# Kernel tuning notes

Hardware: AMD Instinct MI355X
Metric: run time of the kernel (lower is better)

The kernel has to match this reference:

```python
import jax, jax.numpy as jnp
import numpy as np

N, NFEAT, NHID1, NHID2, NCLASS = 16384, 512, 256, 128, 8


def setup_inputs() -> dict:
    key = jax.random.key(0)
    ks = jax.random.split(key, 8)
    x = jax.random.normal(ks[0], (N, NFEAT), dtype=jnp.float32)
    adj = jax.random.uniform(ks[1], (N, N), dtype=jnp.float32)
    W1 = jax.random.normal(ks[2], (NFEAT, NHID1), dtype=jnp.float32) * (1.0 / np.sqrt(NFEAT))
    b1 = jnp.zeros((NHID1,), dtype=jnp.float32)
    W2 = jax.random.normal(ks[3], (NHID1, NHID2), dtype=jnp.float32) * (1.0 / np.sqrt(NHID1))
    b2 = jnp.zeros((NHID2,), dtype=jnp.float32)
    W3 = jax.random.normal(ks[4], (NHID2, NCLASS), dtype=jnp.float32) * (1.0 / np.sqrt(NHID2))
    b3 = jnp.zeros((NCLASS,), dtype=jnp.float32)
    return {"x": x, "adj": adj, "W1": W1, "b1": b1, "W2": W2, "b2": b2, "W3": W3, "b3": b3}


def _gc(x, adj, W, b):
    # GraphConvolution (Kipf): support = x @ W; out = adj @ support + b
    return adj @ (x @ W) + b


def reference(x, adj, W1, b1, W2, b2, W3, b3):
    # eval mode: dropout is identity
    h = jax.nn.relu(_gc(x, adj, W1, b1))
    h = jax.nn.relu(_gc(h, adj, W2, b2))
    h = _gc(h, adj, W3, b3)
    return jax.nn.log_softmax(h, axis=1)
```

## Files before the change

kernel.cpp:

```cpp
#include <hip/hip_runtime.h>
#include <hip/hip_bf16.h>

#define NROW 16384
#define NFEATC 512
#define NH1 256
#define NH2 128
#define NCLS 8

typedef __attribute__((ext_vector_type(8))) short short8;
typedef __attribute__((ext_vector_type(4))) float f32x4;

__device__ __forceinline__ ushort f2bf(float f) {
  union { float f; unsigned u; } v; v.f = f;
  unsigned r = v.u + 0x7FFFu + ((v.u >> 16) & 1u);
  return (ushort)(r >> 16);
}
__device__ __forceinline__ float bf2f(ushort h) {
  union { unsigned u; float f; } v; v.u = ((unsigned)h) << 16; return v.f;
}

__device__ __forceinline__ void gl_lds16(const ushort* g, ushort* l) {
  __builtin_amdgcn_global_load_lds(
      (const __attribute__((address_space(1))) unsigned int*)g,
      (__attribute__((address_space(3))) unsigned int*)l, 16, 0, 0);
}

__global__ __launch_bounds__(256) void transpose_conv(
    const float* __restrict__ in, ushort* __restrict__ out, int K, int N) {
  int idx = blockIdx.x * 256 + threadIdx.x;
  if (idx < K * N) {
    int k = idx / N, n = idx % N;
    out[(size_t)n * K + k] = f2bf(in[idx]);
  }
}

template<int BM, int BN, int WM, int WN, int KSPLIT, bool AFP32, int OUTM, bool WADJ, int MINW>
__global__ __launch_bounds__(256, MINW) void gemm_pipe(
    const void* __restrict__ Ap, const ushort* __restrict__ BT,
    void* __restrict__ Outp, ushort* __restrict__ adjBF,
    const float* __restrict__ bias,
    const int nm, const int nn, const int M, const int N, const int K)
{
  constexpr int BK = 64, LDSK = BK + 8;
  constexpr int MR = WM / 16, NR = WN / 16;
  constexpr int nWc = BN / WN;
  static_assert((BM / WM) * (BN / WN) == 4, "4 waves");
  constexpr int AELEM = BM * BK / 256, ATPR = BK / AELEM;
  constexpr int BELEM = BN * BK / 256, BTPR = BK / BELEM;
  constexpr int A4s = AFP32 ? AELEM / 4 : 1;
  constexpr int A8s = AFP32 ? 1 : AELEM / 8;
  constexpr int B8s = (BELEM >= 8) ? BELEM / 8 : 1;

  __shared__ ushort As[2][BM * LDSK];
  __shared__ ushort Bs[2][BN * LDSK];

  const int t = threadIdx.x, l = t & 63, wid = t >> 6;
  const int wr0 = (wid / nWc) * WM, wc0 = (wid % nWc) * WN;

  const int cpx = gridDim.x >> 3;
  const int flat = (blockIdx.x & 7) * cpx + (blockIdx.x >> 3);
  const int n_blk = flat % nn;
  const int m_blk = (flat / nn) % nm;
  const int ksl = flat / (nn * nm);
  const int bm0 = m_blk * BM, bn0 = n_blk * BN;
  const int kper = K / KSPLIT, kbase = ksl * kper;
  const int NT = kper / BK;

  const int ar = t / ATPR, ak = (t % ATPR) * AELEM;
  const int br = t / BTPR, bk = (t % BTPR) * BELEM;

  const float*  Af = (const float*)Ap + (size_t)(bm0 + ar) * K + kbase + ak;
  const ushort* Ab = (const ushort*)Ap + (size_t)(bm0 + ar) * K + kbase + ak;
  const ushort* Bp = BT + (size_t)(bn0 + br) * K + kbase + bk;
  ushort* adjW = WADJ ? (adjBF + (size_t)(bm0 + ar) * K + kbase + ak) : nullptr;
  const bool wbf = WADJ && (n_blk == 0);

  f32x4 acc[MR][NR] = {};

  float4 aF[A4s];
  short8 aB[A8s];
  short8 bV[B8s];
  ushort4 b4;

  auto loadRegs = [&](int it) {
    const int ko = it * BK;
    if constexpr (AFP32) {
      #pragma unroll
      for (int c = 0; c < A4s; c++) aF[c] = *(const float4*)(Af + ko + 4 * c);
    } else {
      #pragma unroll
      for (int c = 0; c < A8s; c++) aB[c] = *(const short8*)(Ab + ko + 8 * c);
    }
    if constexpr (BELEM >= 8) {
      #pragma unroll
      for (int c = 0; c < B8s; c++) bV[c] = *(const short8*)(Bp + ko + 8 * c);
    } else {
      b4 = *(const ushort4*)(Bp + ko);
    }
  };

  auto writeLds = [&](int buf, int it) {
    const int ko = it * BK;
    if constexpr (AFP32) {
      #pragma unroll
      for (int c = 0; c < A4s; c++) {
        ushort4 v;
        v.x = f2bf(aF[c].x); v.y = f2bf(aF[c].y);
        v.z = f2bf(aF[c].z); v.w = f2bf(aF[c].w);
        *(ushort4*)&As[buf][ar * LDSK + ak + 4 * c] = v;
        if (wbf) *(ushort4*)(adjW + ko + 4 * c) = v;
      }
    } else {
      #pragma unroll
      for (int c = 0; c < A8s; c++)
        *(short8*)&As[buf][ar * LDSK + ak + 8 * c] = aB[c];
    }
    if constexpr (BELEM >= 8) {
      #pragma unroll
      for (int c = 0; c < B8s; c++)
        *(short8*)&Bs[buf][br * LDSK + bk + 8 * c] = bV[c];
    } else {
      *(ushort4*)&Bs[buf][br * LDSK + bk] = b4;
    }
  };

  auto compute = [&](int buf) {
    const int rr = l & 15;
    #pragma unroll
    for (int kk = 0; kk < 2; kk++) {
      const int kb = kk * 32 + (l >> 4) * 8;
      short8 af[MR], bfv[NR];
      #pragma unroll
      for (int m = 0; m < MR; m++)
        af[m] = *(short8*)&As[buf][(wr0 + m * 16 + rr) * LDSK + kb];
      #pragma unroll
      for (int n = 0; n < NR; n++)
        bfv[n] = *(short8*)&Bs[buf][(wc0 + n * 16 + rr) * LDSK + kb];
      #pragma unroll
      for (int m = 0; m < MR; m++)
        #pragma unroll
        for (int n = 0; n < NR; n++)
          acc[m][n] = __builtin_amdgcn_mfma_f32_16x16x32_bf16(af[m], bfv[n], acc[m][n], 0, 0, 0);
    }
  };

  loadRegs(0);
  writeLds(0, 0);
  __syncthreads();
  for (int it = 0; it < NT; it++) {
    const int cur = it & 1;
    if (it + 1 < NT) loadRegs(it + 1);
    compute(cur);
    if (it + 1 < NT) writeLds(cur ^ 1, it + 1);
    __syncthreads();
  }

  #pragma unroll
  for (int m = 0; m < MR; m++) {
    const int row = bm0 + wr0 + m * 16 + (l >> 4) * 4;
    #pragma unroll
    for (int n = 0; n < NR; n++) {
      const int col = bn0 + wc0 + n * 16 + (l & 15);
      if constexpr (OUTM == 1) {
        ushort4 v;
        v.x = f2bf(acc[m][n][0]); v.y = f2bf(acc[m][n][1]);
        v.z = f2bf(acc[m][n][2]); v.w = f2bf(acc[m][n][3]);
        *(ushort4*)((ushort*)Outp + (size_t)col * M + row) = v;
      } else if constexpr (OUTM == 2) {
        float* o = (float*)Outp + (size_t)ksl * M * N;
        #pragma unroll
        for (int r = 0; r < 4; r++)
          o[(size_t)(row + r) * N + col] = acc[m][n][r];
      } else {
        const float bv = bias[col];
        ushort* o = (ushort*)Outp;
        #pragma unroll
        for (int r = 0; r < 4; r++)
          o[(size_t)(row + r) * N + col] = f2bf(fmaxf(acc[m][n][r] + bv, 0.0f));
      }
    }
  }
}

template<int BN, int KSPLIT, int MINW>
__global__ __launch_bounds__(256, MINW) void gemm_lds(
    const ushort* __restrict__ A, const ushort* __restrict__ BT,
    float* __restrict__ part, const int nm, const int M, const int N, const int K)
{
  constexpr int BM = 128, BK = 64;
  constexpr int WM = (BN >= 64) ? 64 : 32;
  constexpr int WN = (BN >= 64) ? 64 : BN;
  constexpr int MR = WM / 16, NR = WN / 16;
  constexpr int nWc = BN / WN;
  __shared__ ushort As[BM * BK];
  __shared__ ushort Bs[BN * BK];

  const int t = threadIdx.x, l = t & 63, wid = t >> 6;
  const int rr = l & 15, hi = l >> 4, r7 = rr & 7;
  const int rin = l >> 3, cin = l & 7;
  const int wr0 = (wid / nWc) * WM, wc0 = (wid % nWc) * WN;

  const int cpx = gridDim.x >> 3;
  const int flat = (blockIdx.x & 7) * cpx + (blockIdx.x >> 3);
  const int m_blk = flat % nm;
  const int ksl  = flat / nm;
  const int bm0 = m_blk * BM;
  const int kper = K / KSPLIT, kbase = ksl * kper;
  const int NT = kper / BK;

  f32x4 acc[MR][NR] = {};

  const int scol = 8 * (cin ^ rin);
  const ushort* Arow[4];
  #pragma unroll
  for (int a = 0; a < 4; a++) {
    const int row = (wid * 4 + a) * 8 + rin;
    Arow[a] = A + (size_t)(bm0 + row) * K + kbase + scol;
  }
  const ushort* Brow[(BN == 128) ? 4 : 1];
  if constexpr (BN == 128) {
    #pragma unroll
    for (int a = 0; a < 4; a++) {
      const int row = (wid * 4 + a) * 8 + rin;
      Brow[a] = BT + (size_t)row * K + kbase + scol;
    }
  } else {
    const int row = wid * 8 + rin;
    Brow[0] = BT + (size_t)row * K + kbase + scol;
  }

  for (int it = 0; it < NT; it++) {
    const int ko = it * BK;
    #pragma unroll
    for (int a = 0; a < 4; a++)
      gl_lds16(Arow[a] + ko, &As[(wid * 4 + a) * 512]);
    if constexpr (BN == 128) {
      #pragma unroll
      for (int a = 0; a < 4; a++)
        gl_lds16(Brow[a] + ko, &Bs[(wid * 4 + a) * 512]);
    } else {
      if (wid < 2) gl_lds16(Brow[0] + ko, &Bs[wid * 512]);
    }
    __syncthreads();
    #pragma unroll
    for (int kk = 0; kk < 2; kk++) {
      const int cof = 8 * ((kk * 4 + hi) ^ r7);
      short8 af[MR], bfv[NR];
      #pragma unroll
      for (int m = 0; m < MR; m++)
        af[m] = *(const short8*)&As[(wr0 + m * 16 + rr) * 64 + cof];
      #pragma unroll
      for (int n = 0; n < NR; n++)
        bfv[n] = *(const short8*)&Bs[(wc0 + n * 16 + rr) * 64 + cof];
      #pragma unroll
      for (int m = 0; m < MR; m++)
        #pragma unroll
        for (int n = 0; n < NR; n++)
          acc[m][n] = __builtin_amdgcn_mfma_f32_16x16x32_bf16(af[m], bfv[n], acc[m][n], 0, 0, 0);
    }
    __syncthreads();
  }

  float* o = part + (size_t)ksl * M * N;
  #pragma unroll
  for (int m = 0; m < MR; m++) {
    const int row = bm0 + wr0 + m * 16 + hi * 4;
    #pragma unroll
    for (int n = 0; n < NR; n++) {
      const int col = wc0 + n * 16 + rr;
      #pragma unroll
      for (int r = 0; r < 4; r++)
        o[(size_t)(row + r) * N + col] = acc[m][n][r];
    }
  }
}

__global__ __launch_bounds__(256) void reduce_relu(
    const float* __restrict__ part, const float* __restrict__ bias,
    ushort* __restrict__ out, const int MN, const int N, const int KS) {
  const int i4 = (blockIdx.x * 256 + threadIdx.x) * 4;
  if (i4 >= MN) return;
  float4 s = *(const float4*)(part + i4);
  for (int k = 1; k < KS; k++) {
    float4 p = *(const float4*)(part + (size_t)k * MN + i4);
    s.x += p.x; s.y += p.y; s.z += p.z; s.w += p.w;
  }
  const int col = i4 % N;
  float4 b = *(const float4*)(bias + col);
  ushort4 v;
  v.x = f2bf(fmaxf(s.x + b.x, 0.0f));
  v.y = f2bf(fmaxf(s.y + b.y, 0.0f));
  v.z = f2bf(fmaxf(s.z + b.z, 0.0f));
  v.w = f2bf(fmaxf(s.w + b.w, 0.0f));
  *(ushort4*)(out + i4) = v;
}

__global__ __launch_bounds__(64) void mm_small(
    const ushort* __restrict__ h2, const float* __restrict__ W3,
    ushort* __restrict__ s3T) {
  __shared__ float w[NH2 * NCLS];
  for (int i = threadIdx.x; i < NH2 * NCLS; i += 64) w[i] = W3[i];
  __syncthreads();
  const int m = blockIdx.x * 64 + threadIdx.x;
  float acc[8] = {};
  const ushort* row = h2 + (size_t)m * NH2;
  #pragma unroll
  for (int c = 0; c < NH2 / 8; c++) {
    short8 v = *(const short8*)(row + c * 8);
    #pragma unroll
    for (int j = 0; j < 8; j++) {
      float h = bf2f((ushort)v[j]);
      const int k = c * 8 + j;
      #pragma unroll
      for (int n = 0; n < 8; n++) acc[n] += h * w[k * 8 + n];
    }
  }
  #pragma unroll
  for (int n = 0; n < 8; n++) s3T[(size_t)n * NROW + m] = f2bf(acc[n]);
  #pragma unroll
  for (int n = 8; n < 16; n++) s3T[(size_t)n * NROW + m] = 0;
}

__global__ __launch_bounds__(256) void final_reduce(
    const float* __restrict__ part, const float* __restrict__ b3,
    float* __restrict__ out) {
  const int m = blockIdx.x * 256 + threadIdx.x;
  float4 s0 = make_float4(0, 0, 0, 0), s1 = make_float4(0, 0, 0, 0);
  #pragma unroll
  for (int k = 0; k < 4; k++) {
    const float4* p = (const float4*)(part + ((size_t)k * NROW + m) * 16);
    float4 a = p[0], b = p[1];
    s0.x += a.x; s0.y += a.y; s0.z += a.z; s0.w += a.w;
    s1.x += b.x; s1.y += b.y; s1.z += b.z; s1.w += b.w;
  }
  float v[8];
  v[0] = s0.x + b3[0]; v[1] = s0.y + b3[1]; v[2] = s0.z + b3[2]; v[3] = s0.w + b3[3];
  v[4] = s1.x + b3[4]; v[5] = s1.y + b3[5]; v[6] = s1.z + b3[6]; v[7] = s1.w + b3[7];
  float mx = v[0];
  #pragma unroll
  for (int n = 1; n < 8; n++) mx = fmaxf(mx, v[n]);
  float s = 0.0f;
  #pragma unroll
  for (int n = 0; n < 8; n++) s += expf(v[n] - mx);
  const float lse = logf(s) + mx;
  float4* o = (float4*)(out + (size_t)m * 8);
  o[0] = make_float4(v[0] - lse, v[1] - lse, v[2] - lse, v[3] - lse);
  o[1] = make_float4(v[4] - lse, v[5] - lse, v[6] - lse, v[7] - lse);
}

extern "C" void kernel_launch(void* const* d_in, const int* in_sizes, int n_in,
                              void* d_out, int out_size, void* d_ws, size_t ws_size,
                              hipStream_t stream) {
  const float* x   = (const float*)d_in[0];
  const float* adj = (const float*)d_in[1];
  const float* W1  = (const float*)d_in[2];
  const float* b1  = (const float*)d_in[3];
  const float* W2  = (const float*)d_in[4];
  const float* b2  = (const float*)d_in[5];
  const float* W3  = (const float*)d_in[6];
  const float* b3  = (const float*)d_in[7];
  float* out = (float*)d_out;

  char* ws = (char*)d_ws;
  size_t off = 0;
  ushort* W1T = (ushort*)(ws + off); off += (size_t)NH1 * NFEATC * 2;
  ushort* W2T = (ushort*)(ws + off); off += (size_t)NH2 * NH1 * 2;
  ushort* s1T = (ushort*)(ws + off); off += (size_t)NH1 * NROW * 2;
  ushort* h1  = (ushort*)(ws + off); off += (size_t)NROW * NH1 * 2;
  ushort* s2T = (ushort*)(ws + off); off += (size_t)NH2 * NROW * 2;
  ushort* h2  = (ushort*)(ws + off); off += (size_t)NROW * NH2 * 2;
  ushort* s3T = (ushort*)(ws + off); off += (size_t)16 * NROW * 2;
  float*  part = (float*)(ws + off); off += (size_t)4 * NROW * NH2 * 4;
  ushort* adjBF = (ushort*)(ws + off); off += (size_t)NROW * NROW * 2;

  transpose_conv<<<(NFEATC * NH1 + 255) / 256, 256, 0, stream>>>(W1, W1T, NFEATC, NH1);
  transpose_conv<<<(NH1 * NH2 + 255) / 256, 256, 0, stream>>>(W2, W2T, NH1, NH2);

  gemm_pipe<64, 128, 32, 64, 1, true, 1, false, 2><<<512, 256, 0, stream>>>(
      x, W1T, s1T, nullptr, nullptr, 256, 2, NROW, NH1, NFEATC);
  gemm_pipe<128, 128, 64, 64, 2, true, 2, true, 2><<<512, 256, 0, stream>>>(
      adj, s1T, part, adjBF, nullptr, 128, 2, NROW, NH1, NROW);
  reduce_relu<<<NROW * NH1 / 4 / 256, 256, 0, stream>>>(
      part, b1, h1, NROW * NH1, NH1, 2);
  gemm_pipe<64, 128, 32, 64, 1, false, 1, false, 2><<<256, 256, 0, stream>>>(
      h1, W2T, s2T, nullptr, nullptr, 256, 1, NROW, NH2, NH1);
  gemm_lds<128, 4, 4><<<512, 256, 0, stream>>>(
      adjBF, s2T, part, 128, NROW, NH2, NROW);
  reduce_relu<<<NROW * NH2 / 4 / 256, 256, 0, stream>>>(
      part, b2, h2, NROW * NH2, NH2, 4);
  mm_small<<<NROW / 64, 64, 0, stream>>>(h2, W3, s3T);
  gemm_lds<16, 4, 4><<<512, 256, 0, stream>>>(
      adjBF, s3T, part, 128, NROW, 16, NROW);
  final_reduce<<<NROW / 256, 256, 0, stream>>>(part, b3, out);
}
```

Before: 894.9 us.

## Double-buffer LDS in adjacency GEMMs, add dedicated fp32-adj convert GEMM, reverse K order

Replaces the generic fp32 adjacency GEMM with a specialized gemm_cvt kernel. It uses swizzled LDS, async global-to-LDS loads for the B operand, and wider 16-byte bf16 stores of the converted adjacency. The gemm_lds kernels become double-buffered with prefetch of the next K tile, and the layer-2 pass walks K in reverse to reuse adjacency data still in cache from the previous pass. The layer-3 pass doubles its K split to 8 with more blocks, so final_reduce sums 8 partials. The aim is to overlap loads with MFMA work and improve L2/MALL reuse, at the cost of more LDS per block and lower occupancy.

```diff
diff --git a/kernel.cpp b/kernel.cpp
--- a/kernel.cpp
+++ b/kernel.cpp
@@ -34,11 +34,10 @@
   }
 }
 
-template<int BM, int BN, int WM, int WN, int KSPLIT, bool AFP32, int OUTM, bool WADJ, int MINW>
+template<int BM, int BN, int WM, int WN, int KSPLIT, bool AFP32, int OUTM, int MINW>
 __global__ __launch_bounds__(256, MINW) void gemm_pipe(
     const void* __restrict__ Ap, const ushort* __restrict__ BT,
-    void* __restrict__ Outp, ushort* __restrict__ adjBF,
-    const float* __restrict__ bias,
+    void* __restrict__ Outp, const float* __restrict__ bias,
     const int nm, const int nn, const int M, const int N, const int K)
 {
   constexpr int BK = 64, LDSK = BK + 8;
@@ -72,8 +71,6 @@
   const float*  Af = (const float*)Ap + (size_t)(bm0 + ar) * K + kbase + ak;
   const ushort* Ab = (const ushort*)Ap + (size_t)(bm0 + ar) * K + kbase + ak;
   const ushort* Bp = BT + (size_t)(bn0 + br) * K + kbase + bk;
-  ushort* adjW = WADJ ? (adjBF + (size_t)(bm0 + ar) * K + kbase + ak) : nullptr;
-  const bool wbf = WADJ && (n_blk == 0);
 
   f32x4 acc[MR][NR] = {};
 
@@ -99,8 +96,7 @@
     }
   };
 
-  auto writeLds = [&](int buf, int it) {
-    const int ko = it * BK;
+  auto writeLds = [&](int buf) {
     if constexpr (AFP32) {
       #pragma unroll
       for (int c = 0; c < A4s; c++) {
@@ -108,7 +104,6 @@
         v.x = f2bf(aF[c].x); v.y = f2bf(aF[c].y);
         v.z = f2bf(aF[c].z); v.w = f2bf(aF[c].w);
         *(ushort4*)&As[buf][ar * LDSK + ak + 4 * c] = v;
-        if (wbf) *(ushort4*)(adjW + ko + 4 * c) = v;
       }
     } else {
       #pragma unroll
@@ -145,13 +140,13 @@
   };
 
   loadRegs(0);
-  writeLds(0, 0);
+  writeLds(0);
   __syncthreads();
   for (int it = 0; it < NT; it++) {
     const int cur = it & 1;
     if (it + 1 < NT) loadRegs(it + 1);
     compute(cur);
-    if (it + 1 < NT) writeLds(cur ^ 1, it + 1);
+    if (it + 1 < NT) writeLds(cur ^ 1);
     __syncthreads();
   }
 
@@ -166,11 +161,6 @@
         v.x = f2bf(acc[m][n][0]); v.y = f2bf(acc[m][n][1]);
         v.z = f2bf(acc[m][n][2]); v.w = f2bf(acc[m][n][3]);
         *(ushort4*)((ushort*)Outp + (size_t)col * M + row) = v;
-      } else if constexpr (OUTM == 2) {
-        float* o = (float*)Outp + (size_t)ksl * M * N;
-        #pragma unroll
-        for (int r = 0; r < 4; r++)
-          o[(size_t)(row + r) * N + col] = acc[m][n][r];
       } else {
         const float bv = bias[col];
         ushort* o = (ushort*)Outp;
@@ -182,8 +172,8 @@
   }
 }
 
-template<int BN, int KSPLIT, int MINW>
-__global__ __launch_bounds__(256, MINW) void gemm_lds(
+template<int BN, int KSPLIT, bool KREV, int MINW>
+__global__ __launch_bounds__(256, MINW) void gemm_lds2(
     const ushort* __restrict__ A, const ushort* __restrict__ BT,
     float* __restrict__ part, const int nm, const int M, const int N, const int K)
 {
@@ -192,8 +182,8 @@
   constexpr int WN = (BN >= 64) ? 64 : BN;
   constexpr int MR = WM / 16, NR = WN / 16;
   constexpr int nWc = BN / WN;
-  __shared__ ushort As[BM * BK];
-  __shared__ ushort Bs[BN * BK];
+  __shared__ ushort As[2][BM * BK];
+  __shared__ ushort Bs[2][BN * BK];
 
   const int t = threadIdx.x, l = t & 63, wid = t >> 6;
   const int rr = l & 15, hi = l >> 4, r7 = rr & 7;
@@ -203,7 +193,7 @@
   const int cpx = gridDim.x >> 3;
   const int flat = (blockIdx.x & 7) * cpx + (blockIdx.x >> 3);
   const int m_blk = flat % nm;
-  const int ksl  = flat / nm;
+  const int ksl = flat / nm;
   const int bm0 = m_blk * BM;
   const int kper = K / KSPLIT, kbase = ksl * kper;
   const int NT = kper / BK;
@@ -213,51 +203,55 @@
   const int scol = 8 * (cin ^ rin);
   const ushort* Arow[4];
   #pragma unroll
+  for (int a = 0; a < 4; a++)
+    Arow[a] = A + (size_t)(bm0 + (wid * 4 + a) * 8 + rin) * K + kbase + scol;
+  const ushort* Brow[4];
+  #pragma unroll
   for (int a = 0; a < 4; a++) {
-    const int row = (wid * 4 + a) * 8 + rin;
-    Arow[a] = A + (size_t)(bm0 + row) * K + kbase + scol;
-  }
-  const ushort* Brow[(BN == 128) ? 4 : 1];
-  if constexpr (BN == 128) {
-    #pragma unroll
-    for (int a = 0; a < 4; a++) {
-      const int row = (wid * 4 + a) * 8 + rin;
-      Brow[a] = BT + (size_t)row * K + kbase + scol;
-    }
-  } else {
-    const int row = wid * 8 + rin;
-    Brow[0] = BT + (size_t)row * K + kbase + scol;
-  }
-
-  for (int it = 0; it < NT; it++) {
-    const int ko = it * BK;
+    int row = (BN == 128) ? ((wid * 4 + a) * 8 + rin) : (wid * 8 + rin);
+    if (row >= BN) row = 0;
+    Brow[a] = BT + (size_t)row * K + kbase + scol;
+  }
+
+  auto STAGE = [&](int buf, int it) {
+    const int ko = (KREV ? (NT - 1 - it) : it) * BK;
     #pragma unroll
     for (int a = 0; a < 4; a++)
-      gl_lds16(Arow[a] + ko, &As[(wid * 4 + a) * 512]);
+      gl_lds16(Arow[a] + ko, &As[buf][(wid * 4 + a) * 512]);
     if constexpr (BN == 128) {
       #pragma unroll
       for (int a = 0; a < 4; a++)
-        gl_lds16(Brow[a] + ko, &Bs[(wid * 4 + a) * 512]);
+        gl_lds16(Brow[a] + ko, &Bs[buf][(wid * 4 + a) * 512]);
     } else {
-      if (wid < 2) gl_lds16(Brow[0] + ko, &Bs[wid * 512]);
-    }
-    __syncthreads();
+      if (wid < 2) gl_lds16(Brow[0] + ko, &Bs[buf][wid * 512]);
+    }
+  };
+
+  auto COMPUTE = [&](int buf) {
     #pragma unroll
     for (int kk = 0; kk < 2; kk++) {
       const int cof = 8 * ((kk * 4 + hi) ^ r7);
       short8 af[MR], bfv[NR];
       #pragma unroll
       for (int m = 0; m < MR; m++)
-        af[m] = *(const short8*)&As[(wr0 + m * 16 + rr) * 64 + cof];
+        af[m] = *(const short8*)&As[buf][(wr0 + m * 16 + rr) * 64 + cof];
       #pragma unroll
       for (int n = 0; n < NR; n++)
-        bfv[n] = *(const short8*)&Bs[(wc0 + n * 16 + rr) * 64 + cof];
+        bfv[n] = *(const short8*)&Bs[buf][(wc0 + n * 16 + rr) * 64 + cof];
       #pragma unroll
       for (int m = 0; m < MR; m++)
         #pragma unroll
         for (int n = 0; n < NR; n++)
           acc[m][n] = __builtin_amdgcn_mfma_f32_16x16x32_bf16(af[m], bfv[n], acc[m][n], 0, 0, 0);
     }
+  };
+
+  STAGE(0, 0);
+  __syncthreads();
+  for (int it = 0; it < NT; it++) {
+    const int cur = it & 1;
+    if (it + 1 < NT) STAGE(cur ^ 1, it + 1);
+    COMPUTE(cur);
     __syncthreads();
   }
 
@@ -271,6 +265,109 @@
       #pragma unroll
       for (int r = 0; r < 4; r++)
         o[(size_t)(row + r) * N + col] = acc[m][n][r];
+    }
+  }
+}
+
+__global__ __launch_bounds__(256, 2) void gemm_cvt(
+    const float* __restrict__ adj, const ushort* __restrict__ BT,
+    float* __restrict__ part, ushort* __restrict__ adjBF)
+{
+  constexpr int BM = 128, BN = 128, BK = 64, MR = 4, NR = 4;
+  __shared__ ushort As[2][BM * BK];
+  __shared__ ushort Bs[2][BN * BK];
+
+  const int t = threadIdx.x, l = t & 63, wid = t >> 6;
+  const int rr = l & 15, hi = l >> 4, r7 = rr & 7;
+  const int rin = l >> 3, cin = l & 7;
+  const int wr0 = (wid >> 1) * 64, wc0 = (wid & 1) * 64;
+
+  const int cpx = gridDim.x >> 3;
+  const int flat = (blockIdx.x & 7) * cpx + (blockIdx.x >> 3);
+  const int n_blk = flat & 1;
+  const int m_blk = (flat >> 1) & 127;
+  const int ksl = flat >> 8;
+  const int bm0 = m_blk * BM, bn0 = n_blk * BN;
+  const int kbase = ksl * (NROW / 2);
+  constexpr int NT = (NROW / 2) / BK;
+
+  const int ar = t >> 1;
+  const int ac4 = (t & 1) * 4;
+  const float* Af = adj + (size_t)(bm0 + ar) * NROW + kbase + ac4 * 8;
+  ushort* adjW = adjBF + (size_t)(bm0 + ar) * NROW + kbase + ac4 * 8;
+  const bool wbf = (n_blk == 0);
+
+  const int scol = 8 * (cin ^ rin);
+  const ushort* Brow[4];
+  #pragma unroll
+  for (int a = 0; a < 4; a++)
+    Brow[a] = BT + (size_t)(bn0 + (wid * 4 + a) * 8 + rin) * NROW + kbase + scol;
+
+  f32x4 acc[MR][NR] = {};
+  float4 aF[8];
+
+  auto LOADA = [&](int it) {
+    #pragma unroll
+    for (int c = 0; c < 8; c++) aF[c] = *(const float4*)(Af + it * 64 + c * 4);
+  };
+  auto STAGEB = [&](int buf, int it) {
+    #pragma unroll
+    for (int a = 0; a < 4; a++)
+      gl_lds16(Brow[a] + it * 64, &Bs[buf][(wid * 4 + a) * 512]);
+  };
+  auto WRITEA = [&](int buf, int it) {
+    #pragma unroll
+    for (int j = 0; j < 4; j++) {
+      short8 v;
+      v[0] = (short)f2bf(aF[2 * j].x);     v[1] = (short)f2bf(aF[2 * j].y);
+      v[2] = (short)f2bf(aF[2 * j].z);     v[3] = (short)f2bf(aF[2 * j].w);
+      v[4] = (short)f2bf(aF[2 * j + 1].x); v[5] = (short)f2bf(aF[2 * j + 1].y);
+      v[6] = (short)f2bf(aF[2 * j + 1].z); v[7] = (short)f2bf(aF[2 * j + 1].w);
+      *(short8*)&As[buf][ar * 64 + 8 * ((ac4 + j) ^ (ar & 7))] = v;
+      if (wbf) *(short8*)(adjW + it * 64 + j * 8) = v;
+    }
+  };
+  auto COMPUTE = [&](int buf) {
+    #pragma unroll
+    for (int kk = 0; kk < 2; kk++) {
+      const int cof = 8 * ((kk * 4 + hi) ^ r7);
+      short8 af[MR], bfv[NR];
+      #pragma unroll
+      for (int m = 0; m < MR; m++)
+        af[m] = *(const short8*)&As[buf][(wr0 + m * 16 + rr) * 64 + cof];
+      #pragma unroll
+      for (int n = 0; n < NR; n++)
+        bfv[n] = *(const short8*)&Bs[buf][(wc0 + n * 16 + rr) * 64 + cof];
+      #pragma unroll
+      for (int m = 0; m < MR; m++)
+        #pragma unroll
+        for (int n = 0; n < NR; n++)
+          acc[m][n] = __builtin_amdgcn_mfma_f32_16x16x32_bf16(af[m], bfv[n], acc[m][n], 0, 0, 0);
+    }
+  };
+
+  LOADA(0);
+  STAGEB(0, 0);
+  WRITEA(0, 0);
+  __syncthreads();
+  for (int it = 0; it < NT; it++) {
+    const int cur = it & 1;
+    if (it + 1 < NT) { LOADA(it + 1); STAGEB(cur ^ 1, it + 1); }
+    COMPUTE(cur);
+    if (it + 1 < NT) WRITEA(cur ^ 1, it + 1);
+    __syncthreads();
+  }
+
+  float* o = part + (size_t)ksl * NROW * NH1;
+  #pragma unroll
+  for (int m = 0; m < MR; m++) {
+    const int row = bm0 + wr0 + m * 16 + hi * 4;
+    #pragma unroll
+    for (int n = 0; n < NR; n++) {
+      const int col = bn0 + wc0 + n * 16 + rr;
+      #pragma unroll
+      for (int r = 0; r < 4; r++)
+        o[(size_t)(row + r) * NH1 + col] = acc[m][n][r];
     }
   }
 }
@@ -327,7 +424,7 @@
   const int m = blockIdx.x * 256 + threadIdx.x;
   float4 s0 = make_float4(0, 0, 0, 0), s1 = make_float4(0, 0, 0, 0);
   #pragma unroll
-  for (int k = 0; k < 4; k++) {
+  for (int k = 0; k < 8; k++) {
     const float4* p = (const float4*)(part + ((size_t)k * NROW + m) * 16);
     float4 a = p[0], b = p[1];
     s0.x += a.x; s0.y += a.y; s0.z += a.z; s0.w += a.w;
@@ -370,26 +467,25 @@
   ushort* s2T = (ushort*)(ws + off); off += (size_t)NH2 * NROW * 2;
   ushort* h2  = (ushort*)(ws + off); off += (size_t)NROW * NH2 * 2;
   ushort* s3T = (ushort*)(ws + off); off += (size_t)16 * NROW * 2;
-  float*  part = (float*)(ws + off); off += (size_t)4 * NROW * NH2 * 4;
+  float*  part = (float*)(ws + off); off += (size_t)2 * NROW * NH1 * 4;
   ushort* adjBF = (ushort*)(ws + off); off += (size_t)NROW * NROW * 2;
 
   transpose_conv<<<(NFEATC * NH1 + 255) / 256, 256, 0, stream>>>(W1, W1T, NFEATC, NH1);
   transpose_conv<<<(NH1 * NH2 + 255) / 256, 256, 0, stream>>>(W2, W2T, NH1, NH2);
 
-  gemm_pipe<64, 128, 32, 64, 1, true, 1, false, 2><<<512, 256, 0, stream>>>(
-      x, W1T, s1T, nullptr, nullptr, 256, 2, NROW, NH1, NFEATC);
-  gemm_pipe<128, 128, 64, 64, 2, true, 2, true, 2><<<512, 256, 0, stream>>>(
-      adj, s1T, part, adjBF, nullptr, 128, 2, NROW, NH1, NROW);
+  gemm_pipe<64, 128, 32, 64, 1, true, 1, 2><<<512, 256, 0, stream>>>(
+      x, W1T, s1T, nullptr, 256, 2, NROW, NH1, NFEATC);
+  gemm_cvt<<<512, 256, 0, stream>>>(adj, s1T, part, adjBF);
   reduce_relu<<<NROW * NH1 / 4 / 256, 256, 0, stream>>>(
       part, b1, h1, NROW * NH1, NH1, 2);
-  gemm_pipe<64, 128, 32, 64, 1, false, 1, false, 2><<<256, 256, 0, stream>>>(
-      h1, W2T, s2T, nullptr, nullptr, 256, 1, NROW, NH2, NH1);
-  gemm_lds<128, 4, 4><<<512, 256, 0, stream>>>(
+  gemm_pipe<64, 128, 32, 64, 1, false, 1, 2><<<256, 256, 0, stream>>>(
+      h1, W2T, s2T, nullptr, 256, 1, NROW, NH2, NH1);
+  gemm_lds2<128, 4, true, 2><<<512, 256, 0, stream>>>(
       adjBF, s2T, part, 128, NROW, NH2, NROW);
   reduce_relu<<<NROW * NH2 / 4 / 256, 256, 0, stream>>>(
       part, b2, h2, NROW * NH2, NH2, 4);
   mm_small<<<NROW / 64, 64, 0, stream>>>(h2, W3, s3T);
-  gemm_lds<16, 4, 4><<<512, 256, 0, stream>>>(
+  gemm_lds2<16, 8, false, 4><<<1024, 256, 0, stream>>>(
       adjBF, s3T, part, 128, NROW, 16, NROW);
   final_reduce<<<NROW / 256, 256, 0, stream>>>(part, b3, out);
 }
```

Measured after the change: 881.7 us. About the same (-1.5%).
